# Kernel optimization log

Hardware: AMD Instinct MI355X
Metric: run time of the kernel (lower is better)

Reference implementation:

```python
import jax, jax.numpy as jnp
import numpy as np


def setup_inputs() -> dict:
    key = jax.random.key(0)
    k1, k2, k3, k4 = jax.random.split(key, 4)
    N = 100000          # n_users + n_items nodes
    E = 1600000         # nonzeros in normalized adjacency (avg degree 16)
    D = 64              # embedding dim
    edge_row = jnp.sort(jax.random.randint(k1, (E,), 0, N, dtype=jnp.int32))
    edge_col = jax.random.randint(k2, (E,), 0, N, dtype=jnp.int32)
    edge_val = jax.random.uniform(k3, (E,), dtype=jnp.float32)
    embeds = jax.random.normal(k4, (N, D), dtype=jnp.float32)
    return {
        "edge_row": edge_row,
        "edge_col": edge_col,
        "edge_val": edge_val,
        "embeds": embeds,
        "num_nodes": N,
    }


def reference(edge_row, edge_col, edge_val, embeds, num_nodes):
    # out = A @ embeds, A given in COO: A[row[e], col[e]] = val[e]
    gathered = edge_val[:, None] * embeds[edge_col]        # [E, D]
    out = jax.ops.segment_sum(gathered, edge_row, num_segments=num_nodes)  # [N, D]
    return out
```

## Files before the change

kernel.cpp:

```cpp
#include <hip/hip_runtime.h>


#define GCN_D 64

typedef float f4 __attribute__((ext_vector_type(4)));

__global__ __launch_bounds__(256) void prep_kernel(
    const float* __restrict__ embeds,
    unsigned char* __restrict__ ebq,
    float* __restrict__ scale,
    int quant_blocks,
    const int* __restrict__ edge_row, int* __restrict__ row_ptr, int E, int N)
{
    if ((int)blockIdx.x < quant_blocks) {
        const int t   = blockIdx.x * blockDim.x + threadIdx.x;
        const int row = t >> 3;
        if (row >= N) return;
        const int l8 = (threadIdx.x & 7) * 8;

        const f4 a = __builtin_nontemporal_load(
            (const f4*)(embeds + (size_t)row * GCN_D + l8));
        const f4 b = __builtin_nontemporal_load(
            (const f4*)(embeds + (size_t)row * GCN_D + l8 + 4));

        float m = fmaxf(fmaxf(fmaxf(fabsf(a.x), fabsf(a.y)),
                              fmaxf(fabsf(a.z), fabsf(a.w))),
                        fmaxf(fmaxf(fabsf(b.x), fabsf(b.y)),
                              fmaxf(fabsf(b.z), fabsf(b.w))));
        m = fmaxf(m, __shfl_xor(m, 1));
        m = fmaxf(m, __shfl_xor(m, 2));
        m = fmaxf(m, __shfl_xor(m, 4));

        const float inv = (m > 0.f) ? 127.f / m : 0.f;
        const int q0 = (int)rintf(fminf(fmaxf(a.x * inv, -127.f), 127.f)) + 128;
        const int q1 = (int)rintf(fminf(fmaxf(a.y * inv, -127.f), 127.f)) + 128;
        const int q2 = (int)rintf(fminf(fmaxf(a.z * inv, -127.f), 127.f)) + 128;
        const int q3 = (int)rintf(fminf(fmaxf(a.w * inv, -127.f), 127.f)) + 128;
        const int q4 = (int)rintf(fminf(fmaxf(b.x * inv, -127.f), 127.f)) + 128;
        const int q5 = (int)rintf(fminf(fmaxf(b.y * inv, -127.f), 127.f)) + 128;
        const int q6 = (int)rintf(fminf(fmaxf(b.z * inv, -127.f), 127.f)) + 128;
        const int q7 = (int)rintf(fminf(fmaxf(b.w * inv, -127.f), 127.f)) + 128;

        unsigned int p0 =
            (unsigned)q0 | ((unsigned)q1 << 8) | ((unsigned)q2 << 16) | ((unsigned)q3 << 24);
        unsigned int p1 =
            (unsigned)q4 | ((unsigned)q5 << 8) | ((unsigned)q6 << 16) | ((unsigned)q7 << 24);

        unsigned int* dst = (unsigned int*)(ebq + (size_t)row * GCN_D + l8);
        dst[0] = p0;
        dst[1] = p1;
        if ((threadIdx.x & 7) == 0) scale[row] = m * (1.f / 127.f);
    } else {
        const int e = (blockIdx.x - quant_blocks) * blockDim.x + threadIdx.x;
        if (e >= E) return;
        const int r    = edge_row[e];
        const int prev = (e == 0) ? -1 : edge_row[e - 1];
        for (int k = prev + 1; k <= r; ++k) row_ptr[k] = e;
        if (e == E - 1)
            for (int k = r + 1; k <= N; ++k) row_ptr[k] = E;
    }
}

__global__ __launch_bounds__(256) void gcn_row_q8_kernel(
    const int* __restrict__ row_ptr,
    const int* __restrict__ edge_col,
    const float* __restrict__ edge_val,
    const unsigned char* __restrict__ ebq,
    const float* __restrict__ scale,
    float* __restrict__ out,
    int N)
{
    const int tid = blockIdx.x * blockDim.x + threadIdx.x;
    const int row = tid >> 4;
    if (row >= N) return;
    const int db = (threadIdx.x & 15) * 4;

    const int p0 = row_ptr[row];
    const int p1 = row_ptr[row + 1];

    f4    acc  = (f4)0.0f;
    float wsum = 0.0f;
    int k = p0;

    for (; k + 7 < p1; k += 8) {
        int   c[8];
        float v[8];
        #pragma unroll
        for (int j = 0; j < 8; ++j) { c[j] = edge_col[k + j]; v[j] = edge_val[k + j]; }
        unsigned int g[8];
        float        s[8];
        #pragma unroll
        for (int j = 0; j < 8; ++j) {
            g[j] = *(const unsigned int*)(ebq + (size_t)c[j] * GCN_D + db);
            s[j] = scale[c[j]];
        }
        #pragma unroll
        for (int j = 0; j < 8; ++j) {
            const float w = v[j] * s[j];
            acc.x += w * (float)( g[j]        & 0xffu);
            acc.y += w * (float)((g[j] >> 8)  & 0xffu);
            acc.z += w * (float)((g[j] >> 16) & 0xffu);
            acc.w += w * (float)( g[j] >> 24);
            wsum  += w;
        }
    }
    if (k + 3 < p1) {
        int   c[4];
        float v[4];
        #pragma unroll
        for (int j = 0; j < 4; ++j) { c[j] = edge_col[k + j]; v[j] = edge_val[k + j]; }
        unsigned int g[4];
        float        s[4];
        #pragma unroll
        for (int j = 0; j < 4; ++j) {
            g[j] = *(const unsigned int*)(ebq + (size_t)c[j] * GCN_D + db);
            s[j] = scale[c[j]];
        }
        #pragma unroll
        for (int j = 0; j < 4; ++j) {
            const float w = v[j] * s[j];
            acc.x += w * (float)( g[j]        & 0xffu);
            acc.y += w * (float)((g[j] >> 8)  & 0xffu);
            acc.z += w * (float)((g[j] >> 16) & 0xffu);
            acc.w += w * (float)( g[j] >> 24);
            wsum  += w;
        }
        k += 4;
    }
    for (; k < p1; ++k) {
        const int c = edge_col[k];
        const unsigned int g = *(const unsigned int*)(ebq + (size_t)c * GCN_D + db);
        const float w = edge_val[k] * scale[c];
        acc.x += w * (float)( g        & 0xffu);
        acc.y += w * (float)((g >> 8)  & 0xffu);
        acc.z += w * (float)((g >> 16) & 0xffu);
        acc.w += w * (float)( g >> 24);
        wsum  += w;
    }

    acc = acc - 128.0f * wsum;

    __builtin_nontemporal_store(acc, (f4*)(out + (size_t)row * GCN_D + db));
}

extern "C" void kernel_launch(void* const* d_in, const int* in_sizes, int n_in,
                              void* d_out, int out_size, void* d_ws, size_t ws_size,
                              hipStream_t stream) {
    const int*   edge_row = (const int*)d_in[0];
    const int*   edge_col = (const int*)d_in[1];
    const float* edge_val = (const float*)d_in[2];
    const float* embeds   = (const float*)d_in[3];
    float*       out      = (float*)d_out;

    const int E = in_sizes[0];
    const int N = out_size / GCN_D;

    int* row_ptr = (int*)d_ws;
    const size_t sc_off = (((size_t)(N + 1) * 4) + 255) & ~(size_t)255;
    float* scale = (float*)((char*)d_ws + sc_off);
    const size_t q_off = ((sc_off + (size_t)N * 4) + 255) & ~(size_t)255;
    unsigned char* ebq = (unsigned char*)d_ws + q_off;

    const int quant_blocks = (N * 8 + 255) / 256;
    const int rp_blocks    = (E + 255) / 256;
    prep_kernel<<<quant_blocks + rp_blocks, 256, 0, stream>>>(
        embeds, ebq, scale, quant_blocks, edge_row, row_ptr, E, N);

    const int row_blocks = (N * 16 + 255) / 256;
    gcn_row_q8_kernel<<<row_blocks, 256, 0, stream>>>(
        row_ptr, edge_col, edge_val, ebq, scale, out, N);
}
```

Measured before the change: 126.7 us.

## Stage per-block edge columns and prescaled weights in LDS for SpMM

Result: no change. 124.5 us (median of 2 runs) (-1.7%).

```diff
diff --git a/kernel.cpp b/kernel.cpp
--- a/kernel.cpp
+++ b/kernel.cpp
@@ -2,6 +2,7 @@
 
 
 #define GCN_D 64
+#define CHUNK_E 512
 
 typedef float f4 __attribute__((ext_vector_type(4)));
 
@@ -61,7 +62,14 @@
     }
 }
 
-__global__ __launch_bounds__(256) void gcn_row_q8_kernel(
+__device__ __forceinline__ void q8_fma4(unsigned int g, float w, f4& acc) {
+    acc.x += w * (float)( g        & 0xffu);
+    acc.y += w * (float)((g >> 8)  & 0xffu);
+    acc.z += w * (float)((g >> 16) & 0xffu);
+    acc.w += w * (float)( g >> 24);
+}
+
+__global__ __launch_bounds__(256) void gcn_row_q8_lds_kernel(
     const int* __restrict__ row_ptr,
     const int* __restrict__ edge_col,
     const float* __restrict__ edge_val,
@@ -70,77 +78,67 @@
     float* __restrict__ out,
     int N)
 {
-    const int tid = blockIdx.x * blockDim.x + threadIdx.x;
-    const int row = tid >> 4;
-    if (row >= N) return;
-    const int db = (threadIdx.x & 15) * 4;
+    __shared__ int2 ls[CHUNK_E];
 
-    const int p0 = row_ptr[row];
-    const int p1 = row_ptr[row + 1];
+    const int brow0 = blockIdx.x * 16;
+    const int row   = brow0 + (threadIdx.x >> 4);
+    const int db    = (threadIdx.x & 15) * 4;
+    const bool rv   = (row < N);
+
+    const int p0 = rv ? row_ptr[row]     : 0;
+    const int p1 = rv ? row_ptr[row + 1] : 0;
+
+    const int rlast = (brow0 + 16 < N) ? (brow0 + 16) : N;
+    const int r0 = row_ptr[brow0];
+    const int r1 = row_ptr[rlast];
 
     f4    acc  = (f4)0.0f;
     float wsum = 0.0f;
-    int k = p0;
 
-    for (; k + 7 < p1; k += 8) {
-        int   c[8];
-        float v[8];
-        #pragma unroll
-        for (int j = 0; j < 8; ++j) { c[j] = edge_col[k + j]; v[j] = edge_val[k + j]; }
-        unsigned int g[8];
-        float        s[8];
-        #pragma unroll
-        for (int j = 0; j < 8; ++j) {
-            g[j] = *(const unsigned int*)(ebq + (size_t)c[j] * GCN_D + db);
-            s[j] = scale[c[j]];
+    for (int cb = r0; cb < r1; cb += CHUNK_E) {
+        const int ce = (cb + CHUNK_E < r1) ? (cb + CHUNK_E) : r1;
+
+        __syncthreads();
+        for (int i = cb + (int)threadIdx.x; i < ce; i += 256) {
+            const int c = edge_col[i];
+            ls[i - cb] = make_int2(c, __float_as_int(edge_val[i] * scale[c]));
         }
-        #pragma unroll
-        for (int j = 0; j < 8; ++j) {
-            const float w = v[j] * s[j];
-            acc.x += w * (float)( g[j]        & 0xffu);
-            acc.y += w * (float)((g[j] >> 8)  & 0xffu);
-            acc.z += w * (float)((g[j] >> 16) & 0xffu);
-            acc.w += w * (float)( g[j] >> 24);
-            wsum  += w;
+        __syncthreads();
+
+        const int k0 = (p0 > cb) ? p0 : cb;
+        const int ke = (p1 < ce) ? p1 : ce;
+        if (ke > k0) {
+            const int nb   = (ke - k0 + 7) >> 3;
+            const int lmax = ce - cb - 1;
+            for (int b = 0; b < nb; ++b) {
+                const int kb = k0 + b * 8;
+                int   c[8];
+                float w[8];
+                #pragma unroll
+                for (int j = 0; j < 8; ++j) {
+                    int idx = kb + j - cb;
+                    idx = (idx > lmax) ? lmax : idx;
+                    const int2 t = ls[idx];
+                    c[j] = t.x;
+                    w[j] = (kb + j < ke) ? __int_as_float(t.y) : 0.0f;
+                }
+                unsigned g[8];
+                #pragma unroll
+                for (int j = 0; j < 8; ++j)
+                    g[j] = *(const unsigned*)(ebq + (size_t)c[j] * GCN_D + db);
+                #pragma unroll
+                for (int j = 0; j < 8; ++j) {
+                    q8_fma4(g[j], w[j], acc);
+                    wsum += w[j];
+                }
+            }
         }
     }
-    if (k + 3 < p1) {
-        int   c[4];
-        float v[4];
-        #pragma unroll
-        for (int j = 0; j < 4; ++j) { c[j] = edge_col[k + j]; v[j] = edge_val[k + j]; }
-        unsigned int g[4];
-        float        s[4];
-        #pragma unroll
-        for (int j = 0; j < 4; ++j) {
-            g[j] = *(const unsigned int*)(ebq + (size_t)c[j] * GCN_D + db);
-            s[j] = scale[c[j]];
-        }
-        #pragma unroll
-        for (int j = 0; j < 4; ++j) {
-            const float w = v[j] * s[j];
-            acc.x += w * (float)( g[j]        & 0xffu);
-            acc.y += w * (float)((g[j] >> 8)  & 0xffu);
-            acc.z += w * (float)((g[j] >> 16) & 0xffu);
-            acc.w += w * (float)( g[j] >> 24);
-            wsum  += w;
-        }
-        k += 4;
+
+    if (rv) {
+        acc = acc - 128.0f * wsum;
+        __builtin_nontemporal_store(acc, (f4*)(out + (size_t)row * GCN_D + db));
     }
-    for (; k < p1; ++k) {
-        const int c = edge_col[k];
-        const unsigned int g = *(const unsigned int*)(ebq + (size_t)c * GCN_D + db);
-        const float w = edge_val[k] * scale[c];
-        acc.x += w * (float)( g        & 0xffu);
-        acc.y += w * (float)((g >> 8)  & 0xffu);
-        acc.z += w * (float)((g >> 16) & 0xffu);
-        acc.w += w * (float)( g >> 24);
-        wsum  += w;
-    }
-
-    acc = acc - 128.0f * wsum;
-
-    __builtin_nontemporal_store(acc, (f4*)(out + (size_t)row * GCN_D + db));
 }
 
 extern "C" void kernel_launch(void* const* d_in, const int* in_sizes, int n_in,
@@ -166,7 +164,7 @@
     prep_kernel<<<quant_blocks + rp_blocks, 256, 0, stream>>>(
         embeds, ebq, scale, quant_blocks, edge_row, row_ptr, E, N);
 
-    const int row_blocks = (N * 16 + 255) / 256;
-    gcn_row_q8_kernel<<<row_blocks, 256, 0, stream>>>(
+    const int row_blocks = (N + 15) / 16;
+    gcn_row_q8_lds_kernel<<<row_blocks, 256, 0, stream>>>(
         row_ptr, edge_col, edge_val, ebq, scale, out, N);
 }
```
